# Performance work log

Measured on AMD Instinct MI355X. Metric: run time of the kernel, lower is better.

## Reference

```python
import jax, jax.numpy as jnp
import numpy as np

K = 5  # spline kernel size per dim (dim=3 -> 125 kernels)
N1, E1 = 10000, 60000
N2, E2 = 2500, 15000
N3, E3 = 625, 3750
N4, E4 = 160, 960
NC = 4  # num part classes (ShapeNet 'Pistol')


def spline_conv(x, ei, u, W, R, b):
    """SplineConv with degree-1 open B-splines, dim=3, kernel_size=K.
    x: [N, in], ei: [2, E] (src, dst), u: [E, 3] pseudo coords in [0,1],
    W: [K^3, in, out], R: [in, out] root weight, b: [out] bias.
    Mean-normalized neighborhood aggregation (norm=True) + root + bias."""
    src, dst = ei[0], ei[1]
    N, E = x.shape[0], ei.shape[1]
    v = u * (K - 1)
    k0f = jnp.clip(jnp.floor(v), 0.0, K - 2)
    f = v - k0f  # fractional offsets in [0, 1]
    k0 = k0f.astype(jnp.int32)
    # Pre-transform node features by every kernel: z[n, k, o]
    z = jnp.einsum('ni,kio->nko', x, W)
    msg = jnp.zeros((E, W.shape[2]), x.dtype)
    for b0 in (0, 1):
        for b1 in (0, 1):
            for b2 in (0, 1):
                idx = (k0[:, 0] + b0) * K * K + (k0[:, 1] + b1) * K + (k0[:, 2] + b2)
                wgt = ((f[:, 0] if b0 else 1.0 - f[:, 0]) *
                       (f[:, 1] if b1 else 1.0 - f[:, 1]) *
                       (f[:, 2] if b2 else 1.0 - f[:, 2]))
                msg = msg + wgt[:, None] * z[src, idx]
    agg = jax.ops.segment_sum(msg, dst, num_segments=N)
    deg = jax.ops.segment_sum(jnp.ones((E,), x.dtype), dst, num_segments=N)
    return agg / jnp.maximum(deg, 1.0)[:, None] + x @ R + b


def _net(x, u1, u2, u3, u4, w1, r1, b1, w12, r12, b12, w2, r2, b2, w22, r22, b22,
         w3, r3, b3, w32, r32, b32, w4, r4, b4, w42, r42, b42, w5, r5, b5,
         w6, r6, b6, w7, r7, b7, fc1w, fc1b, fc2w, fc2b,
         sk1w, sk1b, sk2w, sk2b, sk3w, sk3b, ei1, ei2, ei3, ei4, c1, c2, c3):
    elu = jax.nn.elu
    h1 = elu(spline_conv(x, ei1, u1, w1, r1, b1))
    h1 = elu(spline_conv(h1, ei1, u1, w12, r12, b12))
    h2 = jnp.concatenate([jax.ops.segment_max(h1, c1, num_segments=N2),
                          jnp.ones((N2, 1), x.dtype)], axis=1)
    h2 = elu(spline_conv(h2, ei2, u2, w2, r2, b2))
    h2 = elu(spline_conv(h2, ei2, u2, w22, r22, b22))
    h3 = jnp.concatenate([jax.ops.segment_max(h2, c2, num_segments=N3),
                          jnp.ones((N3, 1), x.dtype)], axis=1)
    h3 = elu(spline_conv(h3, ei3, u3, w3, r3, b3))
    h3 = elu(spline_conv(h3, ei3, u3, w32, r32, b32))
    h4 = jnp.concatenate([jax.ops.segment_max(h3, c3, num_segments=N4),
                          jnp.ones((N4, 1), x.dtype)], axis=1)
    h4 = elu(spline_conv(h4, ei4, u4, w4, r4, b4))
    h4 = elu(spline_conv(h4, ei4, u4, w42, r42, b42))
    h4 = elu(spline_conv(h4, ei4, u4, w42, r42, b42))  # conv42 applied twice, as in source
    h4 = elu(h4 @ fc1w + fc1b)  # dropout omitted (eval mode)
    g3 = elu(spline_conv(h4[c3] + h3 @ sk3w + sk3b, ei3, u3, w5, r5, b5))
    g2 = elu(spline_conv(g3[c2] + h2 @ sk2w + sk2b, ei2, u2, w6, r6, b6))
    g1 = elu(spline_conv(g2[c1] + h1 @ sk1w + sk1b, ei1, u1, w7, r7, b7))
    return jax.nn.log_softmax(g1 @ fc2w + fc2b, axis=1)


def setup_inputs() -> dict:
    key = jax.random.key(0)
    ks = iter(jax.random.split(key, 96))

    def nrm(shape, s=0.1):
        return jax.random.normal(next(ks), shape, jnp.float32) * s

    def edges(E, N):
        return jax.random.randint(next(ks), (2, E), 0, N, dtype=jnp.int32)

    def clus(Nl, Nn):
        # surjective cluster assignment so every pooled voxel is non-empty
        extra = jax.random.randint(next(ks), (Nl - Nn,), 0, Nn, dtype=jnp.int32)
        return jnp.concatenate([jnp.arange(Nn, dtype=jnp.int32), extra])

    d = {}
    d['x'] = nrm((N1, 1), 1.0)
    d['ei1'], d['u1'] = edges(E1, N1), jax.random.uniform(next(ks), (E1, 3), jnp.float32)
    d['ei2'], d['u2'] = edges(E2, N2), jax.random.uniform(next(ks), (E2, 3), jnp.float32)
    d['ei3'], d['u3'] = edges(E3, N3), jax.random.uniform(next(ks), (E3, 3), jnp.float32)
    d['ei4'], d['u4'] = edges(E4, N4), jax.random.uniform(next(ks), (E4, 3), jnp.float32)
    d['c1'], d['c2'], d['c3'] = clus(N1, N2), clus(N2, N3), clus(N3, N4)
    KK = K ** 3
    for name, cin, cout in [('1', 1, 64), ('12', 64, 64), ('2', 65, 64), ('22', 64, 64),
                            ('3', 65, 64), ('32', 64, 64), ('4', 65, 64), ('42', 64, 64),
                            ('5', 32, 32), ('6', 32, 32), ('7', 32, 32)]:
        d['w' + name] = nrm((KK, cin, cout))
        d['r' + name] = nrm((cin, cout))
        d['b' + name] = jnp.zeros((cout,), jnp.float32)
    d['fc1w'], d['fc1b'] = nrm((64, 32)), jnp.zeros((32,), jnp.float32)
    d['fc2w'], d['fc2b'] = nrm((32, NC)), jnp.zeros((NC,), jnp.float32)
    for s in ('1', '2', '3'):
        d['sk' + s + 'w'] = nrm((64, 32))
        d['sk' + s + 'b'] = jnp.zeros((32,), jnp.float32)
    return d


def reference(x, u1, u2, u3, u4, w1, r1, b1, w12, r12, b12, w2, r2, b2, w22, r22, b22,
              w3, r3, b3, w32, r32, b32, w4, r4, b4, w42, r42, b42, w5, r5, b5,
              w6, r6, b6, w7, r7, b7, fc1w, fc1b, fc2w, fc2b,
              sk1w, sk1b, sk2w, sk2b, sk3w, sk3b, ei1, ei2, ei3, ei4, c1, c2, c3):
    return _net(x, u1, u2, u3, u4, w1, r1, b1, w12, r12, b12, w2, r2, b2, w22, r22, b22,
                w3, r3, b3, w32, r32, b32, w4, r4, b4, w42, r42, b42, w5, r5, b5,
                w6, r6, b6, w7, r7, b7, fc1w, fc1b, fc2w, fc2b,
                sk1w, sk1b, sk2w, sk2b, sk3w, sk3b, ei1, ei2, ei3, ei4, c1, c2, c3)
```

## Files before the change

### kernel.cpp

```cpp
#include <hip/hip_runtime.h>
#include <math.h>


static const int N1 = 10000, E1 = 60000;
static const int N2 = 2500,  E2 = 15000;
static const int N3 = 625,   E3 = 3750;
static const int N4 = 160,   E4 = 960;
static const int NC = 4;
static const int CHUNK = 64;

typedef __attribute__((ext_vector_type(8))) short bfrag;
typedef __attribute__((ext_vector_type(4))) float f32x4;

__device__ __forceinline__ float eluf(float x) { return x > 0.f ? x : expm1f(x); }

__device__ __forceinline__ unsigned short bfc(float f) {
    unsigned u = __float_as_uint(f);
    return (unsigned short)((u + 0x7FFF + ((u >> 16) & 1)) >> 16);
}

struct InitArgs {
    const float* wsrc[10]; unsigned short* wdst[10];
    int cinmat[10], xs_[10], cout[10];
    long welems[10];
    long wtot;
    float* pools[3]; int pM[3];
    float* agg; int aggN4;
    int* preblk; int preN;
    int bB, bC, bD;
};

__global__ __launch_bounds__(256) void init_misc(InitArgs A) {
    const int blk = blockIdx.x, tid = threadIdx.x;
    if (blk < A.bB) {
        const long t = (long)blk * 256 + tid;
        if (t >= A.wtot) return;
        int k = 0;
        while (t >= A.welems[k]) ++k;
        const long i2 = t - (k ? A.welems[k - 1] : 0);
        const int co = A.cout[k], cm = A.cinmat[k], xs = A.xs_[k];
        const int KG = cm >> 3;
        const int o = (int)(i2 % co);
        const long rest = i2 / co;
        const int g8 = (int)(rest % KG);
        const int kk = (int)(rest / KG);
        const float* sp = A.wsrc[k] + ((size_t)kk * xs + g8 * 8) * co + o;
        bfrag bv;
        #pragma unroll
        for (int j = 0; j < 8; ++j) bv[j] = (short)bfc(sp[(size_t)j * co]);
        *(bfrag*)(A.wdst[k] + (((size_t)(kk * KG + g8)) * co + o) * 8) = bv;
    } else if (blk < A.bC) {
        const int t = (blk - A.bB) * 256 + tid;
        if (t >= A.pM[2]) return;
        const int p = (t < A.pM[0]) ? 0 : (t < A.pM[1] ? 1 : 2);
        const int base = p ? A.pM[p - 1] : 0;
        const int i2 = t - base;
        A.pools[p][i2] = (i2 % 65 == 64) ? 1.0f : -INFINITY;
    } else if (blk < A.bD) {
        const int t = (blk - A.bC) * 256 + tid;
        if (t < A.aggN4) ((float4*)A.agg)[t] = make_float4(0.f, 0.f, 0.f, 0.f);
    } else {
        const int t = (blk - A.bD) * 256 + tid;
        if (t < A.preN) A.preblk[t] = 0;
    }
}

struct Levels {
    const float* u[4]; const int* ei[4]; int E[4];
    int nb0[5];
    int cb0[5];
    int mc[4];
    int* ek0[4]; int* hist[4]; int* cursor[4]; float* deg[4];
    int* ck0[4]; int* ccnt[4]; int* perm[4];
};

__global__ __launch_bounds__(256) void prep_conv1(Levels L, const float* __restrict__ x,
                                                  const float* __restrict__ w1,
                                                  float* __restrict__ agg, int nbTot) {
    __shared__ int lh[64];
    const int tid = threadIdx.x;
    if ((int)blockIdx.x < nbTot) {
        int l = 0;
        while (l < 3 && (int)blockIdx.x >= L.nb0[l + 1]) ++l;
        const int bl = blockIdx.x - L.nb0[l];
        if (tid < 64) lh[tid] = 0;
        __syncthreads();
        const int e = bl * 256 + tid;
        if (e < L.E[l]) {
            int b = 0;
            #pragma unroll
            for (int d = 0; d < 3; ++d) {
                const float v = L.u[l][e * 3 + d] * 4.0f;
                const float kf = fminf(fmaxf(floorf(v), 0.f), 3.f);
                b = (b << 2) | (int)kf;
            }
            L.ek0[l][e] = b;
            atomicAdd(&lh[b], 1);
            atomicAdd(&L.deg[l][L.ei[l][L.E[l] + e]], 1.0f);
        }
        __syncthreads();
        if (tid < 64 && lh[tid]) atomicAdd(&L.hist[l][tid], lh[tid]);
    } else {
        const int t = (blockIdx.x - nbTot) * 256 + tid;
        const int e = t >> 6, o = t & 63;
        if (e >= E1) return;
        const int src = L.ei[0][e], dst = L.ei[0][E1 + e];
        float f[3]; int kb = 0;
        #pragma unroll
        for (int d = 0; d < 3; ++d) {
            const float v = L.u[0][e * 3 + d] * 4.0f;
            const float kf = fminf(fmaxf(floorf(v), 0.f), 3.f);
            f[d] = v - kf; kb = kb * 5 + (int)kf;
        }
        float s = 0.f;
        #pragma unroll
        for (int c = 0; c < 8; ++c) {
            const int b0 = (c >> 2) & 1, b1 = (c >> 1) & 1, b2 = c & 1;
            const float wgt = (b0 ? f[0] : 1.f - f[0]) * (b1 ? f[1] : 1.f - f[1]) *
                              (b2 ? f[2] : 1.f - f[2]);
            s += wgt * w1[(size_t)(kb + b0 * 25 + b1 * 5 + b2) * 64 + o];
        }
        atomicAdd(&agg[(size_t)dst * 64 + o], x[src] * s);
    }
}

__global__ __launch_bounds__(256) void fill_scatter_node1(
        Levels L, const float* __restrict__ x, float* __restrict__ agg,
        const float* __restrict__ r1, const float* __restrict__ b1,
        float* __restrict__ h1a, int cbTot, int nbTot) {
    __shared__ int sb[65];
    __shared__ int lh[64], lbase[64];
    const int tid = threadIdx.x;
    const int blk = blockIdx.x;
    if (blk < cbTot) {
        int l = 0;
        while (l < 3 && blk >= L.cb0[l + 1]) ++l;
        if (tid == 0) {
            int cc = 0;
            for (int b = 0; b < 64; ++b) { sb[b] = cc; cc += (L.hist[l][b] + CHUNK - 1) / CHUNK; }
            sb[64] = cc;
        }
        __syncthreads();
        const int c = (blk - L.cb0[l]) * 256 + tid;
        if (c < L.mc[l]) {
            if (c >= sb[64]) { L.ccnt[l][c] = 0; L.ck0[l][c] = 0; }
            else {
                int lo = 0, hi = 64;
                while (hi - lo > 1) { int m = (lo + hi) >> 1; if (sb[m] <= c) lo = m; else hi = m; }
                const int j = c - sb[lo];
                L.ck0[l][c] = lo;
                L.ccnt[l][c] = min(CHUNK, L.hist[l][lo] - j * CHUNK);
            }
        }
    } else if (blk < cbTot + nbTot) {
        const int fb = blk - cbTot;
        int l = 0;
        while (l < 3 && fb >= L.nb0[l + 1]) ++l;
        const int bl = fb - L.nb0[l];
        if (tid == 0) {
            int cc = 0;
            for (int b = 0; b < 64; ++b) { sb[b] = cc; cc += (L.hist[l][b] + CHUNK - 1) / CHUNK; }
        }
        if (tid < 64) lh[tid] = 0;
        __syncthreads();
        const int e = bl * 256 + tid;
        int b = -1, r = 0;
        if (e < L.E[l]) { b = L.ek0[l][e]; r = atomicAdd(&lh[b], 1); }
        __syncthreads();
        if (tid < 64) lbase[tid] = lh[tid] ? atomicAdd(&L.cursor[l][tid], lh[tid]) : 0;
        __syncthreads();
        if (e < L.E[l]) L.perm[l][sb[b] * CHUNK + lbase[b] + r] = e;
    } else {
        const int nb = blk - cbTot - nbTot;
        const int lane = tid & 63;
        const int grp  = tid >> 6;
        const int n = nb * 4 + grp;
        if (n >= N1) return;
        const float d = fmaxf(L.deg[0][n], 1.f);
        const size_t idx = (size_t)n * 64 + lane;
        float s = agg[idx] / d + b1[lane];
        agg[idx] = 0.f;
        s += x[n] * r1[lane];
        h1a[idx] = eluf(s);
    }
}

template<int CINMAT, int COUT, bool HAS_ONES, bool SKIP>
__global__ __launch_bounds__(256) void bucket_gemm(
        const float* __restrict__ x, const int* __restrict__ ei, const float* __restrict__ u,
        const unsigned short* __restrict__ Wt, const float* __restrict__ Wf,
        const int* __restrict__ perm, const int* __restrict__ ck0, const int* __restrict__ ccnt,
        float* __restrict__ agg, int E,
        const float* __restrict__ up, const int* __restrict__ cl,
        const float* __restrict__ hh, const float* __restrict__ skw,
        const float* __restrict__ skb) {
    constexpr int ALDA = CINMAT + 8;
    constexpr int KG   = CINMAT / 8;
    constexpr int NT   = COUT / 16;
    constexpr int HALVES = CINMAT / 32;
    constexpr int XS   = CINMAT + (HAS_ONES ? 1 : 0);
    constexpr int IT   = CINMAT / 4;

    __shared__ unsigned short A0s[64 * ALDA], A1s[64 * ALDA];
    __shared__ float gS[64 * 4], sS[64 * 2];
    __shared__ int srcS[64], dstS[64];
    __shared__ float WonesS[HAS_ONES ? 8 * COUT : 4];

    const int chunk = blockIdx.x;
    const int cnt = ccnt[chunk];
    if (cnt == 0) return;
    const int b = ck0[chunk];
    const int kbase = ((b >> 4) & 3) * 25 + ((b >> 2) & 3) * 5 + (b & 3);
    const int cstart = chunk * CHUNK;
    const int tid = threadIdx.x;

    if (tid < CHUNK) {
        const int e = tid;
        const int pe = (e < cnt) ? perm[cstart + e] : -1;
        int sv = -1, dv = 0;
        float g0 = 0, g1 = 0, g2 = 0, g3 = 0, s0 = 0, s1 = 0;
        if (pe >= 0) {
            sv = ei[pe]; dv = ei[E + pe];
            float f[3];
            #pragma unroll
            for (int d2 = 0; d2 < 3; ++d2) {
                const float v = u[pe * 3 + d2] * 4.f;
                const float kf = fminf(fmaxf(floorf(v), 0.f), 3.f);
                f[d2] = v - kf;
            }
            g0 = (1.f - f[0]) * (1.f - f[1]); g1 = (1.f - f[0]) * f[1];
            g2 = f[0] * (1.f - f[1]);         g3 = f[0] * f[1];
            s0 = 1.f - f[2]; s1 = f[2];
        }
        srcS[e] = sv; dstS[e] = dv;
        gS[e * 4 + 0] = g0; gS[e * 4 + 1] = g1; gS[e * 4 + 2] = g2; gS[e * 4 + 3] = g3;
        sS[e * 2 + 0] = s0; sS[e * 2 + 1] = s1;
    }
    if (HAS_ONES) {
        for (int t2 = tid; t2 < 8 * COUT; t2 += 256) {
            const int c = t2 / COUT, o = t2 % COUT;
            const int koff = ((c >> 2) & 1) * 25 + ((c >> 1) & 1) * 5 + (c & 1);
            WonesS[t2] = Wf[((size_t)(kbase + koff) * XS + CINMAT) * COUT + o];
        }
    }
    __syncthreads();

    {
        const int e  = tid >> 2;
        const int ib = (tid & 3) * IT;
        const int sv = srcS[e];
        const float sc0 = sS[e * 2], sc1 = sS[e * 2 + 1];
        float xv[IT];
        if (SKIP) {
            if (sv >= 0) {
                #pragma unroll
                for (int j = 0; j < IT; ++j) xv[j] = up[(size_t)cl[sv] * 32 + ib + j] + skb[ib + j];
                #pragma unroll 4
                for (int i = 0; i < 64; ++i) {
                    const float hv = hh[(size_t)sv * 64 + i];
                    #pragma unroll
                    for (int j = 0; j < IT; ++j) xv[j] += hv * skw[i * 32 + ib + j];
                }
            } else {
                #pragma unroll
                for (int j = 0; j < IT; ++j) xv[j] = 0.f;
            }
        } else if ((XS & 3) == 0) {
            #pragma unroll
            for (int j = 0; j < IT; j += 4) {
                float4 q = make_float4(0.f, 0.f, 0.f, 0.f);
                if (sv >= 0) q = *(const float4*)&x[(size_t)sv * XS + ib + j];
                xv[j] = q.x; xv[j + 1] = q.y; xv[j + 2] = q.z; xv[j + 3] = q.w;
            }
        } else {
            #pragma unroll
            for (int j = 0; j < IT; ++j) xv[j] = (sv >= 0) ? x[(size_t)sv * XS + ib + j] : 0.f;
        }
        #pragma unroll
        for (int j = 0; j < IT; j += 2) {
            const unsigned p0 = bfc(xv[j] * sc0) | ((unsigned)bfc(xv[j + 1] * sc0) << 16);
            const unsigned p1 = bfc(xv[j] * sc1) | ((unsigned)bfc(xv[j + 1] * sc1) << 16);
            *(unsigned*)&A0s[e * ALDA + ib + j] = p0;
            *(unsigned*)&A1s[e * ALDA + ib + j] = p1;
        }
    }
    __syncthreads();

    const int lane = tid & 63;
    const int wid  = tid >> 6;
    const int m0   = wid * 16;
    const int arow = m0 + (lane & 15);
    const int kg   = lane >> 4;
    const int ocol = lane & 15;

    f32x4 acc[4][NT];
    #pragma unroll
    for (int q = 0; q < 4; ++q)
        #pragma unroll
        for (int nt = 0; nt < NT; ++nt) acc[q][nt] = (f32x4){0.f, 0.f, 0.f, 0.f};

    #pragma unroll
    for (int q = 0; q < 4; ++q) {
        #pragma unroll
        for (int b2 = 0; b2 < 2; ++b2) {
            const unsigned short* Ab = b2 ? A1s : A0s;
            const int koff = (q >> 1) * 25 + (q & 1) * 5 + b2;
            #pragma unroll
            for (int hf = 0; hf < HALVES; ++hf) {
                const bfrag a = *(const bfrag*)(Ab + arow * ALDA + hf * 32 + kg * 8);
                const int krow = (kbase + koff) * KG + hf * 4 + kg;
                #pragma unroll
                for (int nt = 0; nt < NT; ++nt) {
                    const bfrag bb = *(const bfrag*)(Wt + ((size_t)krow * COUT + nt * 16 + ocol) * 8);
                    acc[q][nt] = __builtin_amdgcn_mfma_f32_16x16x32_bf16(a, bb, acc[q][nt], 0, 0, 0);
                }
            }
        }
    }

    const int grp = lane >> 4;
    #pragma unroll
    for (int nt = 0; nt < NT; ++nt) {
        const int o = nt * 16 + ocol;
        float wo[8];
        if (HAS_ONES) {
            #pragma unroll
            for (int c = 0; c < 8; ++c) wo[c] = WonesS[c * COUT + o];
        }
        #pragma unroll
        for (int r = 0; r < 4; ++r) {
            const int e = m0 + grp * 4 + r;
            if (e < cnt) {
                const float g0 = gS[e * 4 + 0], g1 = gS[e * 4 + 1];
                const float g2 = gS[e * 4 + 2], g3 = gS[e * 4 + 3];
                float v = g0 * acc[0][nt][r] + g1 * acc[1][nt][r] +
                          g2 * acc[2][nt][r] + g3 * acc[3][nt][r];
                if (HAS_ONES) {
                    const float s0v = sS[e * 2], s1v = sS[e * 2 + 1];
                    v += g0 * (s0v * wo[0] + s1v * wo[1]) + g1 * (s0v * wo[2] + s1v * wo[3]) +
                         g2 * (s0v * wo[4] + s1v * wo[5]) + g3 * (s0v * wo[6] + s1v * wo[7]);
                }
                atomicAdd(&agg[(size_t)dstS[e] * COUT + o], v);
            }
        }
    }
}

enum { NODE_PLAIN = 0, NODE_SEGMAX = 1, NODE_FC1 = 2, NODE_LSM = 3 };

template<int CIN, int COUT, int MODE, bool SKIPIN>
__global__ void spline_node_f(const float* __restrict__ x, float* __restrict__ agg,
                              const float* __restrict__ deg, const float* __restrict__ R,
                              const float* __restrict__ b, float* __restrict__ out, int N,
                              const int* __restrict__ cl, float* __restrict__ pool,
                              const float* __restrict__ fw, const float* __restrict__ fb2,
                              float* __restrict__ fout,
                              const int* __restrict__ skcl, const float* __restrict__ skup,
                              const float* __restrict__ skh, const float* __restrict__ skww,
                              const float* __restrict__ skbb) {
    constexpr int NPB = 256 / COUT;
    __shared__ float rowbuf[NPB][COUT];
    const int lane = threadIdx.x % COUT;
    const int grp  = threadIdx.x / COUT;
    const int n = blockIdx.x * NPB + grp;
    if (n >= N) return;
    const float d = fmaxf(deg[n], 1.f);
    const size_t idx = (size_t)n * COUT + lane;
    float s = agg[idx] / d + b[lane];
    agg[idx] = 0.f;
    if (SKIPIN) {
        float vi = skup[(size_t)skcl[n] * 32 + lane] + skbb[lane];
        #pragma unroll 4
        for (int i = 0; i < 64; ++i) vi += skh[(size_t)n * 64 + i] * skww[i * 32 + lane];
        const int half = threadIdx.x & 32;
        #pragma unroll
        for (int i = 0; i < 32; ++i)
            s += __shfl(vi, half + i, 64) * R[i * 32 + lane];
    } else {
        const float* xs = x + (size_t)n * CIN;
        #pragma unroll 4
        for (int i = 0; i < CIN; ++i) s += xs[i] * R[i * COUT + lane];
    }
    const float val = eluf(s);
    if (MODE == NODE_PLAIN || MODE == NODE_SEGMAX) out[idx] = val;
    if (MODE == NODE_SEGMAX) {
        float* addr = pool + (size_t)cl[n] * 65 + lane;
        if (val >= 0.f) atomicMax((int*)addr, __float_as_int(val));
        else            atomicMin((unsigned int*)addr, __float_as_uint(val));
    }
    if (MODE == NODE_FC1) {
        rowbuf[grp][lane] = val;
        if (lane < 32) {
            float s2 = fb2[lane];
            #pragma unroll 4
            for (int i = 0; i < 64; ++i) s2 += rowbuf[grp][i] * fw[i * 32 + lane];
            fout[(size_t)n * 32 + lane] = eluf(s2);
        }
    }
    if (MODE == NODE_LSM) {
        float p[NC];
        #pragma unroll
        for (int o = 0; o < NC; ++o) p[o] = val * fw[lane * NC + o];
        #pragma unroll
        for (int m = 16; m >= 1; m >>= 1)
            #pragma unroll
            for (int o = 0; o < NC; ++o) p[o] += __shfl_xor(p[o], m, 32);
        #pragma unroll
        for (int o = 0; o < NC; ++o) p[o] += fb2[o];
        const float mx = fmaxf(fmaxf(p[0], p[1]), fmaxf(p[2], p[3]));
        float se = 0.f;
        #pragma unroll
        for (int o = 0; o < NC; ++o) se += expf(p[o] - mx);
        const float lg = logf(se);
        if (lane < NC) fout[(size_t)n * NC + lane] = p[lane] - mx - lg;
    }
}

struct HLevel {
    const int* ei; const float* u; int E; int maxchunks;
    int *ek0, *hist, *cursor, *ck0, *ccnt, *perm;
    float* deg;
};

extern "C" void kernel_launch(void* const* d_in, const int* in_sizes, int n_in,
                              void* d_out, int out_size, void* d_ws, size_t ws_size,
                              hipStream_t stream) {
    const float* x    = (const float*)d_in[0];
    const int*   ei1  = (const int*)  d_in[1];
    const float* u1   = (const float*)d_in[2];
    const int*   ei2  = (const int*)  d_in[3];
    const float* u2   = (const float*)d_in[4];
    const int*   ei3  = (const int*)  d_in[5];
    const float* u3   = (const float*)d_in[6];
    const int*   ei4  = (const int*)  d_in[7];
    const float* u4   = (const float*)d_in[8];
    const int*   c1   = (const int*)  d_in[9];
    const int*   c2   = (const int*)  d_in[10];
    const int*   c3   = (const int*)  d_in[11];
    const float *w1  = (const float*)d_in[12], *r1  = (const float*)d_in[13], *b1  = (const float*)d_in[14];
    const float *w12 = (const float*)d_in[15], *r12 = (const float*)d_in[16], *b12 = (const float*)d_in[17];
    const float *w2  = (const float*)d_in[18], *r2  = (const float*)d_in[19], *b2  = (const float*)d_in[20];
    const float *w22 = (const float*)d_in[21], *r22 = (const float*)d_in[22], *b22 = (const float*)d_in[23];
    const float *w3  = (const float*)d_in[24], *r3  = (const float*)d_in[25], *b3  = (const float*)d_in[26];
    const float *w32 = (const float*)d_in[27], *r32 = (const float*)d_in[28], *b32 = (const float*)d_in[29];
    const float *w4  = (const float*)d_in[30], *r4  = (const float*)d_in[31], *b4  = (const float*)d_in[32];
    const float *w42 = (const float*)d_in[33], *r42 = (const float*)d_in[34], *b42 = (const float*)d_in[35];
    const float *w5  = (const float*)d_in[36], *r5  = (const float*)d_in[37], *b5  = (const float*)d_in[38];
    const float *w6  = (const float*)d_in[39], *r6  = (const float*)d_in[40], *b6  = (const float*)d_in[41];
    const float *w7  = (const float*)d_in[42], *r7  = (const float*)d_in[43], *b7  = (const float*)d_in[44];
    const float *fc1w = (const float*)d_in[45], *fc1b = (const float*)d_in[46];
    const float *fc2w = (const float*)d_in[47], *fc2b = (const float*)d_in[48];
    const float *sk1w = (const float*)d_in[49], *sk1b = (const float*)d_in[50];
    const float *sk2w = (const float*)d_in[51], *sk2b = (const float*)d_in[52];
    const float *sk3w = (const float*)d_in[53], *sk3b = (const float*)d_in[54];
    float* out = (float*)d_out;

    char* wsb = (char*)d_ws;
    size_t off = 0;
    auto alloc = [&](size_t bytes) {
        void* p = wsb + off; off = (off + bytes + 255) & ~(size_t)255; return p;
    };
    auto allocF = [&](size_t n) { return (float*)alloc(n * 4); };
    auto allocI = [&](size_t n) { return (int*)alloc(n * 4); };
    auto allocH = [&](size_t n) { return (unsigned short*)alloc(n * 2); };

    float* h1a  = allocF((size_t)N1 * 64);
    float* h1   = allocF((size_t)N1 * 64);
    float* h2in = allocF((size_t)N2 * 65);
    float* h2a  = allocF((size_t)N2 * 64);
    float* h2   = allocF((size_t)N2 * 64);
    float* h3in = allocF((size_t)N3 * 65);
    float* h3a  = allocF((size_t)N3 * 64);
    float* h3   = allocF((size_t)N3 * 64);
    float* h4in = allocF((size_t)N4 * 65);
    float* h4a  = allocF((size_t)N4 * 64);
    float* h4b  = allocF((size_t)N4 * 64);
    float* h4   = allocF((size_t)N4 * 32);
    float* g3   = allocF((size_t)N3 * 32);
    float* g2   = allocF((size_t)N2 * 32);
    float* agg  = allocF((size_t)N1 * 64);

    const size_t SZ64 = (size_t)125 * 8 * 64 * 8;
    const size_t SZ32 = (size_t)125 * 4 * 32 * 8;
    unsigned short* t12 = allocH(SZ64);
    unsigned short* t22 = allocH(SZ64);
    unsigned short* t32 = allocH(SZ64);
    unsigned short* t42 = allocH(SZ64);
    unsigned short* t2  = allocH(SZ64);
    unsigned short* t3  = allocH(SZ64);
    unsigned short* t4  = allocH(SZ64);
    unsigned short* t5  = allocH(SZ32);
    unsigned short* t6  = allocH(SZ32);
    unsigned short* t7  = allocH(SZ32);

    HLevel L[4];
    const int*   eis[4] = {ei1, ei2, ei3, ei4};
    const float* us [4] = {u1, u2, u3, u4};
    const int    Es [4] = {E1, E2, E3, E4};
    const int    Ns [4] = {N1, N2, N3, N4};

    int preN = 0;
    for (int l = 0; l < 4; ++l) preN += 128 + Ns[l];
    int* preblk = allocI(preN);
    {
        int c = 0;
        for (int l = 0; l < 4; ++l) {
            L[l].ei = eis[l]; L[l].u = us[l]; L[l].E = Es[l];
            L[l].maxchunks = (Es[l] + CHUNK - 1) / CHUNK + 64;
            L[l].hist = preblk + c; L[l].cursor = preblk + c + 64;
            L[l].deg = (float*)(preblk + c + 128);
            c += 128 + Ns[l];
            L[l].ek0     = allocI(Es[l]);
            L[l].ck0     = allocI(L[l].maxchunks);
            L[l].ccnt    = allocI(L[l].maxchunks);
            L[l].perm    = allocI((size_t)L[l].maxchunks * CHUNK);
        }
    }

    InitArgs IA;
    {
        const float* srcs[10] = {w12, w22, w32, w42, w2, w3, w4, w5, w6, w7};
        unsigned short* dsts[10] = {t12, t22, t32, t42, t2, t3, t4, t5, t6, t7};
        const int cms[10] = {64,64,64,64,64,64,64,32,32,32};
        const int xss[10] = {64,64,64,64,65,65,65,32,32,32};
        const int cos[10] = {64,64,64,64,64,64,64,32,32,32};
        long cum = 0;
        for (int k = 0; k < 10; ++k) {
            IA.wsrc[k] = srcs[k]; IA.wdst[k] = dsts[k];
            IA.cinmat[k] = cms[k]; IA.xs_[k] = xss[k]; IA.cout[k] = cos[k];
            cum += (long)125 * (cms[k] / 8) * cos[k];
            IA.welems[k] = cum;
        }
        IA.wtot = cum;
        IA.pools[0] = h2in; IA.pools[1] = h3in; IA.pools[2] = h4in;
        IA.pM[0] = N2 * 65; IA.pM[1] = N2 * 65 + N3 * 65; IA.pM[2] = N2 * 65 + N3 * 65 + N4 * 65;
        IA.agg = agg; IA.aggN4 = N1 * 64 / 4;
        IA.preblk = preblk; IA.preN = preN;
        const int bA = (int)((IA.wtot + 255) / 256);
        const int bB = (IA.pM[2] + 255) / 256;
        const int bC = (IA.aggN4 + 255) / 256;
        const int bD = (preN + 255) / 256;
        IA.bB = bA; IA.bC = bA + bB; IA.bD = bA + bB + bC;
        init_misc<<<bA + bB + bC + bD, 256, 0, stream>>>(IA);
    }

    Levels DL;
    int nbTot = 0, cbTot = 0;
    {
        for (int l = 0; l < 4; ++l) {
            DL.u[l] = L[l].u; DL.ei[l] = L[l].ei; DL.E[l] = L[l].E;
            DL.nb0[l] = nbTot; nbTot += (L[l].E + 255) / 256;
            DL.cb0[l] = cbTot; cbTot += (L[l].maxchunks + 255) / 256;
            DL.mc[l] = L[l].maxchunks;
            DL.ek0[l] = L[l].ek0; DL.hist[l] = L[l].hist; DL.cursor[l] = L[l].cursor;
            DL.deg[l] = L[l].deg;
            DL.ck0[l] = L[l].ck0; DL.ccnt[l] = L[l].ccnt; DL.perm[l] = L[l].perm;
        }
        DL.nb0[4] = nbTot; DL.cb0[4] = cbTot;
        const int conv1B = (E1 * 64) / 256;
        prep_conv1<<<nbTot + conv1B, 256, 0, stream>>>(DL, x, w1, agg, nbTot);
        const int n1B = (N1 + 3) / 4;
        fill_scatter_node1<<<cbTot + nbTot + n1B, 256, 0, stream>>>(
            DL, x, agg, r1, b1, h1a, cbTot, nbTot);
    }

    bucket_gemm<64, 64, false, false><<<L[0].maxchunks, 256, 0, stream>>>(
        h1a, L[0].ei, L[0].u, t12, nullptr, L[0].perm, L[0].ck0, L[0].ccnt, agg, L[0].E,
        nullptr, nullptr, nullptr, nullptr, nullptr);
    spline_node_f<64, 64, NODE_SEGMAX, false><<<(N1 + 3) / 4, 256, 0, stream>>>(
        h1a, agg, L[0].deg, r12, b12, h1, N1, c1, h2in, nullptr, nullptr, nullptr,
        nullptr, nullptr, nullptr, nullptr, nullptr);

    bucket_gemm<64, 64, true, false><<<L[1].maxchunks, 256, 0, stream>>>(
        h2in, L[1].ei, L[1].u, t2, w2, L[1].perm, L[1].ck0, L[1].ccnt, agg, L[1].E,
        nullptr, nullptr, nullptr, nullptr, nullptr);
    spline_node_f<65, 64, NODE_PLAIN, false><<<(N2 + 3) / 4, 256, 0, stream>>>(
        h2in, agg, L[1].deg, r2, b2, h2a, N2, nullptr, nullptr, nullptr, nullptr, nullptr,
        nullptr, nullptr, nullptr, nullptr, nullptr);
    bucket_gemm<64, 64, false, false><<<L[1].maxchunks, 256, 0, stream>>>(
        h2a, L[1].ei, L[1].u, t22, nullptr, L[1].perm, L[1].ck0, L[1].ccnt, agg, L[1].E,
        nullptr, nullptr, nullptr, nullptr, nullptr);
    spline_node_f<64, 64, NODE_SEGMAX, false><<<(N2 + 3) / 4, 256, 0, stream>>>(
        h2a, agg, L[1].deg, r22, b22, h2, N2, c2, h3in, nullptr, nullptr, nullptr,
        nullptr, nullptr, nullptr, nullptr, nullptr);

    bucket_gemm<64, 64, true, false><<<L[2].maxchunks, 256, 0, stream>>>(
        h3in, L[2].ei, L[2].u, t3, w3, L[2].perm, L[2].ck0, L[2].ccnt, agg, L[2].E,
        nullptr, nullptr, nullptr, nullptr, nullptr);
    spline_node_f<65, 64, NODE_PLAIN, false><<<(N3 + 3) / 4, 256, 0, stream>>>(
        h3in, agg, L[2].deg, r3, b3, h3a, N3, nullptr, nullptr, nullptr, nullptr, nullptr,
        nullptr, nullptr, nullptr, nullptr, nullptr);
    bucket_gemm<64, 64, false, false><<<L[2].maxchunks, 256, 0, stream>>>(
        h3a, L[2].ei, L[2].u, t32, nullptr, L[2].perm, L[2].ck0, L[2].ccnt, agg, L[2].E,
        nullptr, nullptr, nullptr, nullptr, nullptr);
    spline_node_f<64, 64, NODE_SEGMAX, false><<<(N3 + 3) / 4, 256, 0, stream>>>(
        h3a, agg, L[2].deg, r32, b32, h3, N3, c3, h4in, nullptr, nullptr, nullptr,
        nullptr, nullptr, nullptr, nullptr, nullptr);

    bucket_gemm<64, 64, true, false><<<L[3].maxchunks, 256, 0, stream>>>(
        h4in, L[3].ei, L[3].u, t4, w4, L[3].perm, L[3].ck0, L[3].ccnt, agg, L[3].E,
        nullptr, nullptr, nullptr, nullptr, nullptr);
    spline_node_f<65, 64, NODE_PLAIN, false><<<(N4 + 3) / 4, 256, 0, stream>>>(
        h4in, agg, L[3].deg, r4, b4, h4a, N4, nullptr, nullptr, nullptr, nullptr, nullptr,
        nullptr, nullptr, nullptr, nullptr, nullptr);
    bucket_gemm<64, 64, false, false><<<L[3].maxchunks, 256, 0, stream>>>(
        h4a, L[3].ei, L[3].u, t42, nullptr, L[3].perm, L[3].ck0, L[3].ccnt, agg, L[3].E,
        nullptr, nullptr, nullptr, nullptr, nullptr);
    spline_node_f<64, 64, NODE_PLAIN, false><<<(N4 + 3) / 4, 256, 0, stream>>>(
        h4a, agg, L[3].deg, r42, b42, h4b, N4, nullptr, nullptr, nullptr, nullptr, nullptr,
        nullptr, nullptr, nullptr, nullptr, nullptr);
    bucket_gemm<64, 64, false, false><<<L[3].maxchunks, 256, 0, stream>>>(
        h4b, L[3].ei, L[3].u, t42, nullptr, L[3].perm, L[3].ck0, L[3].ccnt, agg, L[3].E,
        nullptr, nullptr, nullptr, nullptr, nullptr);
    spline_node_f<64, 64, NODE_FC1, false><<<(N4 + 3) / 4, 256, 0, stream>>>(
        h4b, agg, L[3].deg, r42, b42, nullptr, N4, nullptr, nullptr, fc1w, fc1b, h4,
        nullptr, nullptr, nullptr, nullptr, nullptr);

    bucket_gemm<32, 32, false, true><<<L[2].maxchunks, 256, 0, stream>>>(
        nullptr, L[2].ei, L[2].u, t5, nullptr, L[2].perm, L[2].ck0, L[2].ccnt, agg, L[2].E,
        h4, c3, h3, sk3w, sk3b);
    spline_node_f<32, 32, NODE_PLAIN, true><<<(N3 + 7) / 8, 256, 0, stream>>>(
        nullptr, agg, L[2].deg, r5, b5, g3, N3, nullptr, nullptr, nullptr, nullptr, nullptr,
        c3, h4, h3, sk3w, sk3b);

    bucket_gemm<32, 32, false, true><<<L[1].maxchunks, 256, 0, stream>>>(
        nullptr, L[1].ei, L[1].u, t6, nullptr, L[1].perm, L[1].ck0, L[1].ccnt, agg, L[1].E,
        g3, c2, h2, sk2w, sk2b);
    spline_node_f<32, 32, NODE_PLAIN, true><<<(N2 + 7) / 8, 256, 0, stream>>>(
        nullptr, agg, L[1].deg, r6, b6, g2, N2, nullptr, nullptr, nullptr, nullptr, nullptr,
        c2, g3, h2, sk2w, sk2b);

    bucket_gemm<32, 32, false, true><<<L[0].maxchunks, 256, 0, stream>>>(
        nullptr, L[0].ei, L[0].u, t7, nullptr, L[0].perm, L[0].ck0, L[0].ccnt, agg, L[0].E,
        g2, c1, h1, sk1w, sk1b);
    spline_node_f<32, 32, NODE_LSM, true><<<(N1 + 7) / 8, 256, 0, stream>>>(
        nullptr, agg, L[0].deg, r7, b7, nullptr, N1, nullptr, nullptr, fc2w, fc2b, out,
        c1, g2, h1, sk1w, sk1b);
}
```

Before: 294.9 us.

## Fuse node finalization into bucket GEMM via per-node countdown completion

Each conv layer's separate node kernel (normalize, root transform, bias, ELU, pooling/FC epilogues) is folded into the edge GEMM kernel. A per-node remaining-edge counter (deg+1) is decremented atomically after each chunk's scatter, and whichever block brings it to zero runs the node epilogue. Extra blocks cover isolated nodes. The skip-connection transform moves out of the per-edge GEMM gather into a separate per-node skip_gather kernel, so it is computed once per node rather than per edge. This removes about a dozen kernel launches and the extra passes over agg. In exchange it adds atomic traffic, fences, and serialized per-wave epilogue work, and it relies on correct memory ordering between atomic scatters and the finishing block.

```diff
diff --git a/kernel.cpp b/kernel.cpp
--- a/kernel.cpp
+++ b/kernel.cpp
@@ -66,12 +66,13 @@
 }
 
 struct Levels {
-    const float* u[4]; const int* ei[4]; int E[4];
+    const float* u[4]; const int* ei[4]; int E[4]; int Na[4];
     int nb0[5];
     int cb0[5];
+    int rb0[5];
     int mc[4];
     int* ek0[4]; int* hist[4]; int* cursor[4]; float* deg[4];
-    int* ck0[4]; int* ccnt[4]; int* perm[4];
+    int* ck0[4]; int* ccnt[4]; int* perm[4]; int* rem[4];
 };
 
 __global__ __launch_bounds__(256) void prep_conv1(Levels L, const float* __restrict__ x,
@@ -127,7 +128,7 @@
 __global__ __launch_bounds__(256) void fill_scatter_node1(
         Levels L, const float* __restrict__ x, float* __restrict__ agg,
         const float* __restrict__ r1, const float* __restrict__ b1,
-        float* __restrict__ h1a, int cbTot, int nbTot) {
+        float* __restrict__ h1a, int cbTot, int nbTot, int n1B) {
     __shared__ int sb[65];
     __shared__ int lh[64], lbase[64];
     const int tid = threadIdx.x;
@@ -170,7 +171,7 @@
         if (tid < 64) lbase[tid] = lh[tid] ? atomicAdd(&L.cursor[l][tid], lh[tid]) : 0;
         __syncthreads();
         if (e < L.E[l]) L.perm[l][sb[b] * CHUNK + lbase[b] + r] = e;
-    } else {
+    } else if (blk < cbTot + nbTot + n1B) {
         const int nb = blk - cbTot - nbTot;
         const int lane = tid & 63;
         const int grp  = tid >> 6;
@@ -182,18 +183,82 @@
         agg[idx] = 0.f;
         s += x[n] * r1[lane];
         h1a[idx] = eluf(s);
-    }
-}
-
-template<int CINMAT, int COUT, bool HAS_ONES, bool SKIP>
-__global__ __launch_bounds__(256) void bucket_gemm(
+    } else {
+        const int rb = blk - cbTot - nbTot - n1B;
+        int l = 0;
+        while (l < 3 && rb >= L.rb0[l + 1]) ++l;
+        const int n = (rb - L.rb0[l]) * 256 + tid;
+        if (n < L.Na[l]) L.rem[l][n] = (int)L.deg[l][n] + 1;
+    }
+}
+
+enum { M_PLAIN = 0, M_SEGMAX = 1, M_FC1 = 2, M_LSM = 3 };
+
+template<int COUT, int XS, int MODE>
+__device__ __forceinline__ void finish_node(
+        int n, const float* __restrict__ x, float* __restrict__ agg,
+        const float* __restrict__ deg, const float* __restrict__ R,
+        const float* __restrict__ bb, float* __restrict__ outp,
+        const int* __restrict__ cl, float* __restrict__ pool,
+        const float* __restrict__ fw, const float* __restrict__ fb2,
+        float* __restrict__ fout, int* __restrict__ rem) {
+    const int lane = threadIdx.x & 63;
+    const float dr = deg[n];
+    const float d = fmaxf(dr, 1.f);
+    float val = 0.f;
+    if (COUT == 64 || lane < 32) {
+        const size_t idx = (size_t)n * COUT + lane;
+        float s = __hip_atomic_load(&agg[idx], __ATOMIC_RELAXED, __HIP_MEMORY_SCOPE_AGENT) / d
+                  + bb[lane];
+        __hip_atomic_store(&agg[idx], 0.f, __ATOMIC_RELAXED, __HIP_MEMORY_SCOPE_AGENT);
+        const float* xs = x + (size_t)n * XS;
+        #pragma unroll 4
+        for (int i = 0; i < XS; ++i) s += xs[i] * R[i * COUT + lane];
+        val = eluf(s);
+        if (MODE == M_PLAIN || MODE == M_SEGMAX) outp[idx] = val;
+        if (MODE == M_SEGMAX) {
+            float* addr = pool + (size_t)cl[n] * 65 + lane;
+            if (val >= 0.f) atomicMax((int*)addr, __float_as_int(val));
+            else            atomicMin((unsigned int*)addr, __float_as_uint(val));
+        }
+        if (MODE == M_LSM) {
+            float p[NC];
+            #pragma unroll
+            for (int o = 0; o < NC; ++o) p[o] = val * fw[lane * NC + o];
+            #pragma unroll
+            for (int m = 16; m >= 1; m >>= 1)
+                #pragma unroll
+                for (int o = 0; o < NC; ++o) p[o] += __shfl_xor(p[o], m, 32);
+            #pragma unroll
+            for (int o = 0; o < NC; ++o) p[o] += fb2[o];
+            const float mx = fmaxf(fmaxf(p[0], p[1]), fmaxf(p[2], p[3]));
+            float se = 0.f;
+            #pragma unroll
+            for (int o = 0; o < NC; ++o) se += expf(p[o] - mx);
+            const float lg = logf(se);
+            if (lane < NC) fout[(size_t)n * NC + lane] = p[lane] - mx - lg;
+        }
+    }
+    if (MODE == M_FC1) {
+        float s2 = fb2[lane & 31];
+        #pragma unroll 4
+        for (int i = 0; i < 64; ++i) s2 += __shfl(val, i, 64) * fw[i * 32 + (lane & 31)];
+        if (lane < 32) fout[(size_t)n * 32 + lane] = eluf(s2);
+    }
+    if (lane == 0)
+        __hip_atomic_store(&rem[n], (int)dr + 1, __ATOMIC_RELAXED, __HIP_MEMORY_SCOPE_AGENT);
+}
+
+template<int CINMAT, int COUT, bool HAS_ONES, int MODE>
+__global__ __launch_bounds__(256) void bucket_gemm_f(
         const float* __restrict__ x, const int* __restrict__ ei, const float* __restrict__ u,
         const unsigned short* __restrict__ Wt, const float* __restrict__ Wf,
         const int* __restrict__ perm, const int* __restrict__ ck0, const int* __restrict__ ccnt,
-        float* __restrict__ agg, int E,
-        const float* __restrict__ up, const int* __restrict__ cl,
-        const float* __restrict__ hh, const float* __restrict__ skw,
-        const float* __restrict__ skb) {
+        float* __restrict__ agg, int E, int mc, int N,
+        int* __restrict__ rem, const float* __restrict__ deg,
+        const float* __restrict__ R, const float* __restrict__ bb, float* __restrict__ outp,
+        const int* __restrict__ cl, float* __restrict__ pool,
+        const float* __restrict__ fw, const float* __restrict__ fb2, float* __restrict__ fout) {
     constexpr int ALDA = CINMAT + 8;
     constexpr int KG   = CINMAT / 8;
     constexpr int NT   = COUT / 16;
@@ -201,18 +266,35 @@
     constexpr int XS   = CINMAT + (HAS_ONES ? 1 : 0);
     constexpr int IT   = CINMAT / 4;
 
+    const int blk = blockIdx.x;
+    const int tid = threadIdx.x;
+
+    if (blk >= mc) {
+        const int wid = tid >> 6, lane = tid & 63;
+        const int base = (blk - mc) * 256 + wid * 64;
+        const int n = base + lane;
+        bool win = false;
+        if (n < N) win = (atomicSub(&rem[n], 1) == 1);
+        unsigned long long wm = __ballot(win);
+        while (wm) {
+            const int i = __ffsll(wm) - 1;
+            wm &= wm - 1;
+            finish_node<COUT, XS, MODE>(base + i, x, agg, deg, R, bb, outp,
+                                        cl, pool, fw, fb2, fout, rem);
+        }
+        return;
+    }
+
     __shared__ unsigned short A0s[64 * ALDA], A1s[64 * ALDA];
     __shared__ float gS[64 * 4], sS[64 * 2];
     __shared__ int srcS[64], dstS[64];
     __shared__ float WonesS[HAS_ONES ? 8 * COUT : 4];
 
-    const int chunk = blockIdx.x;
-    const int cnt = ccnt[chunk];
+    const int cnt = ccnt[blk];
     if (cnt == 0) return;
-    const int b = ck0[chunk];
+    const int b = ck0[blk];
     const int kbase = ((b >> 4) & 3) * 25 + ((b >> 2) & 3) * 5 + (b & 3);
-    const int cstart = chunk * CHUNK;
-    const int tid = threadIdx.x;
+    const int cstart = blk * CHUNK;
 
     if (tid < CHUNK) {
         const int e = tid;
@@ -251,21 +333,7 @@
         const int sv = srcS[e];
         const float sc0 = sS[e * 2], sc1 = sS[e * 2 + 1];
         float xv[IT];
-        if (SKIP) {
-            if (sv >= 0) {
-                #pragma unroll
-                for (int j = 0; j < IT; ++j) xv[j] = up[(size_t)cl[sv] * 32 + ib + j] + skb[ib + j];
-                #pragma unroll 4
-                for (int i = 0; i < 64; ++i) {
-                    const float hv = hh[(size_t)sv * 64 + i];
-                    #pragma unroll
-                    for (int j = 0; j < IT; ++j) xv[j] += hv * skw[i * 32 + ib + j];
-                }
-            } else {
-                #pragma unroll
-                for (int j = 0; j < IT; ++j) xv[j] = 0.f;
-            }
-        } else if ((XS & 3) == 0) {
+        if ((XS & 3) == 0) {
             #pragma unroll
             for (int j = 0; j < IT; j += 4) {
                 float4 q = make_float4(0.f, 0.f, 0.f, 0.f);
@@ -311,8 +379,8 @@
                 const int krow = (kbase + koff) * KG + hf * 4 + kg;
                 #pragma unroll
                 for (int nt = 0; nt < NT; ++nt) {
-                    const bfrag bb = *(const bfrag*)(Wt + ((size_t)krow * COUT + nt * 16 + ocol) * 8);
-                    acc[q][nt] = __builtin_amdgcn_mfma_f32_16x16x32_bf16(a, bb, acc[q][nt], 0, 0, 0);
+                    const bfrag bbv = *(const bfrag*)(Wt + ((size_t)krow * COUT + nt * 16 + ocol) * 8);
+                    acc[q][nt] = __builtin_amdgcn_mfma_f32_16x16x32_bf16(a, bbv, acc[q][nt], 0, 0, 0);
                 }
             }
         }
@@ -344,81 +412,38 @@
             }
         }
     }
-}
-
-enum { NODE_PLAIN = 0, NODE_SEGMAX = 1, NODE_FC1 = 2, NODE_LSM = 3 };
-
-template<int CIN, int COUT, int MODE, bool SKIPIN>
-__global__ void spline_node_f(const float* __restrict__ x, float* __restrict__ agg,
-                              const float* __restrict__ deg, const float* __restrict__ R,
-                              const float* __restrict__ b, float* __restrict__ out, int N,
-                              const int* __restrict__ cl, float* __restrict__ pool,
-                              const float* __restrict__ fw, const float* __restrict__ fb2,
-                              float* __restrict__ fout,
-                              const int* __restrict__ skcl, const float* __restrict__ skup,
-                              const float* __restrict__ skh, const float* __restrict__ skww,
-                              const float* __restrict__ skbb) {
-    constexpr int NPB = 256 / COUT;
-    __shared__ float rowbuf[NPB][COUT];
-    const int lane = threadIdx.x % COUT;
-    const int grp  = threadIdx.x / COUT;
-    const int n = blockIdx.x * NPB + grp;
+
+    __syncthreads();
+    __threadfence();
+    const int e4 = wid * 16 + lane;
+    bool win = false;
+    if (lane < 16 && e4 < cnt) win = (atomicSub(&rem[dstS[e4]], 1) == 1);
+    unsigned long long wm = __ballot(win);
+    while (wm) {
+        const int i = __ffsll(wm) - 1;
+        wm &= wm - 1;
+        finish_node<COUT, XS, MODE>(dstS[wid * 16 + i], x, agg, deg, R, bb, outp,
+                                    cl, pool, fw, fb2, fout, rem);
+    }
+}
+
+__global__ void skip_gather(const float* __restrict__ up, const int* __restrict__ cl,
+                            const float* __restrict__ h, const float* __restrict__ skw,
+                            const float* __restrict__ skb, float* __restrict__ out, int N) {
+    const int lane = threadIdx.x & 31;
+    const int grp  = threadIdx.x >> 5;
+    const int n = blockIdx.x * 8 + grp;
     if (n >= N) return;
-    const float d = fmaxf(deg[n], 1.f);
-    const size_t idx = (size_t)n * COUT + lane;
-    float s = agg[idx] / d + b[lane];
-    agg[idx] = 0.f;
-    if (SKIPIN) {
-        float vi = skup[(size_t)skcl[n] * 32 + lane] + skbb[lane];
-        #pragma unroll 4
-        for (int i = 0; i < 64; ++i) vi += skh[(size_t)n * 64 + i] * skww[i * 32 + lane];
-        const int half = threadIdx.x & 32;
-        #pragma unroll
-        for (int i = 0; i < 32; ++i)
-            s += __shfl(vi, half + i, 64) * R[i * 32 + lane];
-    } else {
-        const float* xs = x + (size_t)n * CIN;
-        #pragma unroll 4
-        for (int i = 0; i < CIN; ++i) s += xs[i] * R[i * COUT + lane];
-    }
-    const float val = eluf(s);
-    if (MODE == NODE_PLAIN || MODE == NODE_SEGMAX) out[idx] = val;
-    if (MODE == NODE_SEGMAX) {
-        float* addr = pool + (size_t)cl[n] * 65 + lane;
-        if (val >= 0.f) atomicMax((int*)addr, __float_as_int(val));
-        else            atomicMin((unsigned int*)addr, __float_as_uint(val));
-    }
-    if (MODE == NODE_FC1) {
-        rowbuf[grp][lane] = val;
-        if (lane < 32) {
-            float s2 = fb2[lane];
-            #pragma unroll 4
-            for (int i = 0; i < 64; ++i) s2 += rowbuf[grp][i] * fw[i * 32 + lane];
-            fout[(size_t)n * 32 + lane] = eluf(s2);
-        }
-    }
-    if (MODE == NODE_LSM) {
-        float p[NC];
-        #pragma unroll
-        for (int o = 0; o < NC; ++o) p[o] = val * fw[lane * NC + o];
-        #pragma unroll
-        for (int m = 16; m >= 1; m >>= 1)
-            #pragma unroll
-            for (int o = 0; o < NC; ++o) p[o] += __shfl_xor(p[o], m, 32);
-        #pragma unroll
-        for (int o = 0; o < NC; ++o) p[o] += fb2[o];
-        const float mx = fmaxf(fmaxf(p[0], p[1]), fmaxf(p[2], p[3]));
-        float se = 0.f;
-        #pragma unroll
-        for (int o = 0; o < NC; ++o) se += expf(p[o] - mx);
-        const float lg = logf(se);
-        if (lane < NC) fout[(size_t)n * NC + lane] = p[lane] - mx - lg;
-    }
+    float s = up[(size_t)cl[n] * 32 + lane] + skb[lane];
+    const float* hs = h + (size_t)n * 64;
+    #pragma unroll 4
+    for (int i = 0; i < 64; ++i) s += hs[i] * skw[i * 32 + lane];
+    out[(size_t)n * 32 + lane] = s;
 }
 
 struct HLevel {
-    const int* ei; const float* u; int E; int maxchunks;
-    int *ek0, *hist, *cursor, *ck0, *ccnt, *perm;
+    const int* ei; const float* u; int E; int maxchunks; int N; int vb;
+    int *ek0, *hist, *cursor, *ck0, *ccnt, *perm, *rem;
     float* deg;
 };
 
@@ -476,8 +501,11 @@
     float* h4a  = allocF((size_t)N4 * 64);
     float* h4b  = allocF((size_t)N4 * 64);
     float* h4   = allocF((size_t)N4 * 32);
+    float* g3in = allocF((size_t)N3 * 32);
     float* g3   = allocF((size_t)N3 * 32);
+    float* g2in = allocF((size_t)N2 * 32);
     float* g2   = allocF((size_t)N2 * 32);
+    float* g1in = allocF((size_t)N1 * 32);
     float* agg  = allocF((size_t)N1 * 64);
 
     const size_t SZ64 = (size_t)125 * 8 * 64 * 8;
@@ -505,8 +533,9 @@
     {
         int c = 0;
         for (int l = 0; l < 4; ++l) {
-            L[l].ei = eis[l]; L[l].u = us[l]; L[l].E = Es[l];
+            L[l].ei = eis[l]; L[l].u = us[l]; L[l].E = Es[l]; L[l].N = Ns[l];
             L[l].maxchunks = (Es[l] + CHUNK - 1) / CHUNK + 64;
+            L[l].vb = (Ns[l] + 255) / 256;
             L[l].hist = preblk + c; L[l].cursor = preblk + c + 64;
             L[l].deg = (float*)(preblk + c + 128);
             c += 128 + Ns[l];
@@ -514,6 +543,7 @@
             L[l].ck0     = allocI(L[l].maxchunks);
             L[l].ccnt    = allocI(L[l].maxchunks);
             L[l].perm    = allocI((size_t)L[l].maxchunks * CHUNK);
+            L[l].rem     = allocI(Ns[l]);
         }
     }
 
@@ -545,95 +575,58 @@
     }
 
     Levels DL;
-    int nbTot = 0, cbTot = 0;
+    int nbTot = 0, cbTot = 0, rbTot = 0;
     {
         for (int l = 0; l < 4; ++l) {
-            DL.u[l] = L[l].u; DL.ei[l] = L[l].ei; DL.E[l] = L[l].E;
+            DL.u[l] = L[l].u; DL.ei[l] = L[l].ei; DL.E[l] = L[l].E; DL.Na[l] = L[l].N;
             DL.nb0[l] = nbTot; nbTot += (L[l].E + 255) / 256;
             DL.cb0[l] = cbTot; cbTot += (L[l].maxchunks + 255) / 256;
+            DL.rb0[l] = rbTot; rbTot += L[l].vb;
             DL.mc[l] = L[l].maxchunks;
             DL.ek0[l] = L[l].ek0; DL.hist[l] = L[l].hist; DL.cursor[l] = L[l].cursor;
             DL.deg[l] = L[l].deg;
             DL.ck0[l] = L[l].ck0; DL.ccnt[l] = L[l].ccnt; DL.perm[l] = L[l].perm;
-        }
-        DL.nb0[4] = nbTot; DL.cb0[4] = cbTot;
+            DL.rem[l] = L[l].rem;
+        }
+        DL.nb0[4] = nbTot; DL.cb0[4] = cbTot; DL.rb0[4] = rbTot;
         const int conv1B = (E1 * 64) / 256;
         prep_conv1<<<nbTot + conv1B, 256, 0, stream>>>(DL, x, w1, agg, nbTot);
         const int n1B = (N1 + 3) / 4;
-        fill_scatter_node1<<<cbTot + nbTot + n1B, 256, 0, stream>>>(
-            DL, x, agg, r1, b1, h1a, cbTot, nbTot);
-    }
-
-    bucket_gemm<64, 64, false, false><<<L[0].maxchunks, 256, 0, stream>>>(
-        h1a, L[0].ei, L[0].u, t12, nullptr, L[0].perm, L[0].ck0, L[0].ccnt, agg, L[0].E,
-        nullptr, nullptr, nullptr, nullptr, nullptr);
-    spline_node_f<64, 64, NODE_SEGMAX, false><<<(N1 + 3) / 4, 256, 0, stream>>>(
-        h1a, agg, L[0].deg, r12, b12, h1, N1, c1, h2in, nullptr, nullptr, nullptr,
-        nullptr, nullptr, nullptr, nullptr, nullptr);
-
-    bucket_gemm<64, 64, true, false><<<L[1].maxchunks, 256, 0, stream>>>(
-        h2in, L[1].ei, L[1].u, t2, w2, L[1].perm, L[1].ck0, L[1].ccnt, agg, L[1].E,
-        nullptr, nullptr, nullptr, nullptr, nullptr);
-    spline_node_f<65, 64, NODE_PLAIN, false><<<(N2 + 3) / 4, 256, 0, stream>>>(
-        h2in, agg, L[1].deg, r2, b2, h2a, N2, nullptr, nullptr, nullptr, nullptr, nullptr,
-        nullptr, nullptr, nullptr, nullptr, nullptr);
-    bucket_gemm<64, 64, false, false><<<L[1].maxchunks, 256, 0, stream>>>(
-        h2a, L[1].ei, L[1].u, t22, nullptr, L[1].perm, L[1].ck0, L[1].ccnt, agg, L[1].E,
-        nullptr, nullptr, nullptr, nullptr, nullptr);
-    spline_node_f<64, 64, NODE_SEGMAX, false><<<(N2 + 3) / 4, 256, 0, stream>>>(
-        h2a, agg, L[1].deg, r22, b22, h2, N2, c2, h3in, nullptr, nullptr, nullptr,
-        nullptr, nullptr, nullptr, nullptr, nullptr);
-
-    bucket_gemm<64, 64, true, false><<<L[2].maxchunks, 256, 0, stream>>>(
-        h3in, L[2].ei, L[2].u, t3, w3, L[2].perm, L[2].ck0, L[2].ccnt, agg, L[2].E,
-        nullptr, nullptr, nullptr, nullptr, nullptr);
-    spline_node_f<65, 64, NODE_PLAIN, false><<<(N3 + 3) / 4, 256, 0, stream>>>(
-        h3in, agg, L[2].deg, r3, b3, h3a, N3, nullptr, nullptr, nullptr, nullptr, nullptr,
-        nullptr, nullptr, nullptr, nullptr, nullptr);
-    bucket_gemm<64, 64, false, false><<<L[2].maxchunks, 256, 0, stream>>>(
-        h3a, L[2].ei, L[2].u, t32, nullptr, L[2].perm, L[2].ck0, L[2].ccnt, agg, L[2].E,
-        nullptr, nullptr, nullptr, nullptr, nullptr);
-    spline_node_f<64, 64, NODE_SEGMAX, false><<<(N3 + 3) / 4, 256, 0, stream>>>(
-        h3a, agg, L[2].deg, r32, b32, h3, N3, c3, h4in, nullptr, nullptr, nullptr,
-        nullptr, nullptr, nullptr, nullptr, nullptr);
-
-    bucket_gemm<64, 64, true, false><<<L[3].maxchunks, 256, 0, stream>>>(
-        h4in, L[3].ei, L[3].u, t4, w4, L[3].perm, L[3].ck0, L[3].ccnt, agg, L[3].E,
-        nullptr, nullptr, nullptr, nullptr, nullptr);
-    spline_node_f<65, 64, NODE_PLAIN, false><<<(N4 + 3) / 4, 256, 0, stream>>>(
-        h4in, agg, L[3].deg, r4, b4, h4a, N4, nullptr, nullptr, nullptr, nullptr, nullptr,
-        nullptr, nullptr, nullptr, nullptr, nullptr);
-    bucket_gemm<64, 64, false, false><<<L[3].maxchunks, 256, 0, stream>>>(
-        h4a, L[3].ei, L[3].u, t42, nullptr, L[3].perm, L[3].ck0, L[3].ccnt, agg, L[3].E,
-        nullptr, nullptr, nullptr, nullptr, nullptr);
-    spline_node_f<64, 64, NODE_PLAIN, false><<<(N4 + 3) / 4, 256, 0, stream>>>(
-        h4a, agg, L[3].deg, r42, b42, h4b, N4, nullptr, nullptr, nullptr, nullptr, nullptr,
-        nullptr, nullptr, nullptr, nullptr, nullptr);
-    bucket_gemm<64, 64, false, false><<<L[3].maxchunks, 256, 0, stream>>>(
-        h4b, L[3].ei, L[3].u, t42, nullptr, L[3].perm, L[3].ck0, L[3].ccnt, agg, L[3].E,
-        nullptr, nullptr, nullptr, nullptr, nullptr);
-    spline_node_f<64, 64, NODE_FC1, false><<<(N4 + 3) / 4, 256, 0, stream>>>(
-        h4b, agg, L[3].deg, r42, b42, nullptr, N4, nullptr, nullptr, fc1w, fc1b, h4,
-        nullptr, nullptr, nullptr, nullptr, nullptr);
-
-    bucket_gemm<32, 32, false, true><<<L[2].maxchunks, 256, 0, stream>>>(
-        nullptr, L[2].ei, L[2].u, t5, nullptr, L[2].perm, L[2].ck0, L[2].ccnt, agg, L[2].E,
-        h4, c3, h3, sk3w, sk3b);
-    spline_node_f<32, 32, NODE_PLAIN, true><<<(N3 + 7) / 8, 256, 0, stream>>>(
-        nullptr, agg, L[2].deg, r5, b5, g3, N3, nullptr, nullptr, nullptr, nullptr, nullptr,
-        c3, h4, h3, sk3w, sk3b);
-
-    bucket_gemm<32, 32, false, true><<<L[1].maxchunks, 256, 0, stream>>>(
-        nullptr, L[1].ei, L[1].u, t6, nullptr, L[1].perm, L[1].ck0, L[1].ccnt, agg, L[1].E,
-        g3, c2, h2, sk2w, sk2b);
-    spline_node_f<32, 32, NODE_PLAIN, true><<<(N2 + 7) / 8, 256, 0, stream>>>(
-        nullptr, agg, L[1].deg, r6, b6, g2, N2, nullptr, nullptr, nullptr, nullptr, nullptr,
-        c2, g3, h2, sk2w, sk2b);
-
-    bucket_gemm<32, 32, false, true><<<L[0].maxchunks, 256, 0, stream>>>(
-        nullptr, L[0].ei, L[0].u, t7, nullptr, L[0].perm, L[0].ck0, L[0].ccnt, agg, L[0].E,
-        g2, c1, h1, sk1w, sk1b);
-    spline_node_f<32, 32, NODE_LSM, true><<<(N1 + 7) / 8, 256, 0, stream>>>(
-        nullptr, agg, L[0].deg, r7, b7, nullptr, N1, nullptr, nullptr, fc2w, fc2b, out,
-        c1, g2, h1, sk1w, sk1b);
-}
+        fill_scatter_node1<<<cbTot + nbTot + n1B + rbTot, 256, 0, stream>>>(
+            DL, x, agg, r1, b1, h1a, cbTot, nbTot, n1B);
+    }
+
+    #define GEMMF(CM, CO, HO, MODE, XIN, WT, WF, LV, RR, BB, OUTP, CL, POOL, FW, FB, FOUT) \
+        bucket_gemm_f<CM, CO, HO, MODE><<<L[LV].maxchunks + L[LV].vb, 256, 0, stream>>>(   \
+            XIN, L[LV].ei, L[LV].u, WT, WF, L[LV].perm, L[LV].ck0, L[LV].ccnt, agg,        \
+            L[LV].E, L[LV].maxchunks, L[LV].N, L[LV].rem, L[LV].deg,                       \
+            RR, BB, OUTP, CL, POOL, FW, FB, FOUT)
+
+    GEMMF(64, 64, false, M_SEGMAX, h1a, t12, nullptr, 0, r12, b12, h1, c1, h2in,
+          nullptr, nullptr, nullptr);
+    GEMMF(64, 64, true,  M_PLAIN,  h2in, t2, w2, 1, r2, b2, h2a, nullptr, nullptr,
+          nullptr, nullptr, nullptr);
+    GEMMF(64, 64, false, M_SEGMAX, h2a, t22, nullptr, 1, r22, b22, h2, c2, h3in,
+          nullptr, nullptr, nullptr);
+    GEMMF(64, 64, true,  M_PLAIN,  h3in, t3, w3, 2, r3, b3, h3a, nullptr, nullptr,
+          nullptr, nullptr, nullptr);
+    GEMMF(64, 64, false, M_SEGMAX, h3a, t32, nullptr, 2, r32, b32, h3, c3, h4in,
+          nullptr, nullptr, nullptr);
+    GEMMF(64, 64, true,  M_PLAIN,  h4in, t4, w4, 3, r4, b4, h4a, nullptr, nullptr,
+          nullptr, nullptr, nullptr);
+    GEMMF(64, 64, false, M_PLAIN,  h4a, t42, nullptr, 3, r42, b42, h4b, nullptr, nullptr,
+          nullptr, nullptr, nullptr);
+    GEMMF(64, 64, false, M_FC1,    h4b, t42, nullptr, 3, r42, b42, nullptr, nullptr, nullptr,
+          fc1w, fc1b, h4);
+
+    skip_gather<<<(N3 + 7) / 8, 256, 0, stream>>>(h4, c3, h3, sk3w, sk3b, g3in, N3);
+    GEMMF(32, 32, false, M_PLAIN,  g3in, t5, nullptr, 2, r5, b5, g3, nullptr, nullptr,
+          nullptr, nullptr, nullptr);
+    skip_gather<<<(N2 + 7) / 8, 256, 0, stream>>>(g3, c2, h2, sk2w, sk2b, g2in, N2);
+    GEMMF(32, 32, false, M_PLAIN,  g2in, t6, nullptr, 1, r6, b6, g2, nullptr, nullptr,
+          nullptr, nullptr, nullptr);
+    skip_gather<<<(N1 + 7) / 8, 256, 0, stream>>>(g2, c1, h1, sk1w, sk1b, g1in, N1);
+    GEMMF(32, 32, false, M_LSM,    g1in, t7, nullptr, 0, r7, b7, nullptr, nullptr, nullptr,
+          fc2w, fc2b, out);
+    #undef GEMMF
+}
```

Measured after the change: 864.3 us. 2.93x slower.
